# Kernel optimization log

Measured on AMD Instinct MI355X. Metric: run time of the kernel, lower is better.

## Reference

```python
import jax, jax.numpy as jnp
import numpy as np

TOP_K = 4  # num_experts_per_tok


def setup_inputs() -> dict:
    key = jax.random.key(0)
    ks = jax.random.split(key, 5)
    T, H, M, E = 2048, 1024, 512, 32
    sH = 1.0 / np.sqrt(H)
    sM = 1.0 / np.sqrt(M)
    return {
        "x": jax.random.normal(ks[0], (T, 1, H), dtype=jnp.float32),
        "gate_w": jax.random.normal(ks[1], (E, H), dtype=jnp.float32) * sH,   # router nn.Linear weight [E, H]
        "w_gate": jax.random.normal(ks[2], (E, M, H), dtype=jnp.float32) * sH,  # ffn_gate_exps, per expert [M, H]
        "w_up": jax.random.normal(ks[3], (E, M, H), dtype=jnp.float32) * sH,    # ffn_up_exps
        "w_down": jax.random.normal(ks[4], (E, H, M), dtype=jnp.float32) * sM,  # ffn_down_exps, per expert [H, M]
    }


def reference(x, gate_w, w_gate, w_up, w_down):
    # x: [T, S, H]; only the last position is used (decode path)
    curr = x[:, -1, :]                                   # [T, H]
    T = curr.shape[0]
    E = gate_w.shape[0]

    # router: logits = curr @ gate_w^T, top-k, softmax over top-k logits
    logits = curr @ gate_w.T                             # [T, E]
    topk_vals, topk_ids = jax.lax.top_k(logits, TOP_K)   # [T, K]
    topk_weights = jax.nn.softmax(topk_vals, axis=-1)    # [T, K]

    # dense routing matrix [T, E]: weight for chosen experts, 0 elsewhere
    route = jnp.zeros((T, E), dtype=curr.dtype)
    route = route.at[jnp.arange(T)[:, None], topk_ids].add(topk_weights)

    # expert MLPs: gate/up -> silu(gate)*up -> down, weighted combine
    gate_act = jnp.einsum('th,emh->tem', curr, w_gate)   # [T, E, M]
    up_act = jnp.einsum('th,emh->tem', curr, w_up)
    mixed = jax.nn.silu(gate_act) * up_act * route[:, :, None]
    out = jnp.einsum('tem,ehm->th', mixed, w_down)       # [T, H]

    return out.reshape(T, 1, -1)
```

## Files before the change

kernel.cpp:

```cpp
#include <hip/hip_runtime.h>
#include <math.h>

#define T_TOK 2048
#define H_DIM 1024
#define M_DIM 512
#define E_NUM 32
#define TOPK  4

#define BT  128
#define BK  32
#define GU_BM 64
#define DN_BH 128
#define MAX_TILES 96

typedef __bf16 bf16x8 __attribute__((ext_vector_type(8)));
typedef float f32x4 __attribute__((ext_vector_type(4)));
typedef unsigned short u16x8 __attribute__((ext_vector_type(8)));

__device__ __forceinline__ unsigned short f2bf(float f) {
  unsigned u = __float_as_uint(f);
  return (unsigned short)((u + 0x7fffu + ((u >> 16) & 1u)) >> 16);
}
__device__ __forceinline__ float bf2f(unsigned short h) {
  return __uint_as_float(((unsigned)h) << 16);
}
__device__ __forceinline__ f32x4 mfma16(bf16x8 a, bf16x8 b, f32x4 c) {
  return __builtin_amdgcn_mfma_f32_16x16x32_bf16(a, b, c, 0, 0, 0);
}

__global__ __launch_bounds__(512) void split_x_kernel(
    const float* __restrict__ x, unsigned short* __restrict__ xh,
    unsigned short* __restrict__ xl) {
  int i = (blockIdx.x * 512 + threadIdx.x) * 8;
  float t8[8];
  *(float4*)t8 = *(const float4*)(x + i);
  *(float4*)(t8 + 4) = *(const float4*)(x + i + 4);
  u16x8 hv, lv;
  #pragma unroll
  for (int j = 0; j < 8; ++j) {
    unsigned short h = f2bf(t8[j]);
    hv[j] = h;
    lv[j] = f2bf(t8[j] - bf2f(h));
  }
  *(u16x8*)(xh + i) = hv;
  *(u16x8*)(xl + i) = lv;
}

__global__ __launch_bounds__(256) void gating_kernel(
    const float* __restrict__ x, const float* __restrict__ gate_w,
    int* __restrict__ topk_ids, float* __restrict__ topk_w) {
  __shared__ float xr[H_DIM];
  __shared__ float logits[E_NUM];
  int t = blockIdx.x;
  int tid = threadIdx.x;
  const float* xrow = x + (size_t)t * H_DIM;
  *(float4*)(xr + tid * 4) = *(const float4*)(xrow + tid * 4);
  __syncthreads();
  int wave = tid >> 6, lane = tid & 63;
  const float4* x4 = (const float4*)xr;
  for (int e8 = 0; e8 < 8; ++e8) {
    int e = wave * 8 + e8;
    const float4* g4 = (const float4*)(gate_w + (size_t)e * H_DIM);
    float p = 0.f;
    #pragma unroll
    for (int i = 0; i < 4; ++i) {
      float4 a = x4[lane + i * 64];
      float4 b = g4[lane + i * 64];
      p += a.x * b.x + a.y * b.y + a.z * b.z + a.w * b.w;
    }
    for (int off = 32; off > 0; off >>= 1) p += __shfl_down(p, off, 64);
    if (lane == 0) logits[e] = p;
  }
  __syncthreads();
  if (tid == 0) {
    float v[E_NUM];
    for (int e = 0; e < E_NUM; ++e) v[e] = logits[e];
    int ids[TOPK]; float vals[TOPK];
    for (int k = 0; k < TOPK; ++k) {
      int bi = 0; float bv = -1e30f;
      for (int e = 0; e < E_NUM; ++e) if (v[e] > bv) { bv = v[e]; bi = e; }
      ids[k] = bi; vals[k] = bv; v[bi] = -1e30f;
    }
    float m = vals[0];
    float w[TOPK]; float s = 0.f;
    for (int k = 0; k < TOPK; ++k) { w[k] = expf(vals[k] - m); s += w[k]; }
    float inv = 1.f / s;
    for (int k = 0; k < TOPK; ++k) {
      topk_ids[t * TOPK + k] = ids[k];
      topk_w[t * TOPK + k]   = w[k] * inv;
    }
  }
}

__global__ __launch_bounds__(256) void scatter_kernel(
    const int* __restrict__ topk_ids, int* __restrict__ cursors,
    int* __restrict__ tok_list) {
  int g = blockIdx.x * 256 + threadIdx.x;
  if (g >= T_TOK * TOPK) return;
  int e = topk_ids[g];
  int slot = atomicAdd(&cursors[e], 1);
  tok_list[e * T_TOK + slot] = g;
}

__global__ void build_tiles(const int* __restrict__ cursors,
                            int* __restrict__ n_tiles, int* __restrict__ tile_list) {
  int lane = threadIdx.x;
  int nt = 0;
  if (lane < E_NUM) nt = (cursors[lane] + BT - 1) / BT;
  int pfx = nt;
  for (int off = 1; off < 64; off <<= 1) {
    int v = __shfl_up(pfx, off, 64);
    if (lane >= off) pfx += v;
  }
  int excl = pfx - nt;
  if (lane == E_NUM - 1) *n_tiles = pfx;
  if (lane < E_NUM)
    for (int i = 0; i < nt; ++i) tile_list[excl + i] = (lane << 8) | i;
}

__global__ __launch_bounds__(512) void gateup_mfma(
    const unsigned short* __restrict__ xh, const unsigned short* __restrict__ xl,
    const float* __restrict__ w_gate, const float* __restrict__ w_up,
    const float* __restrict__ topk_w,
    const int* __restrict__ cursors, const int* __restrict__ tok_list,
    const int* __restrict__ n_tiles, const int* __restrict__ tile_list,
    unsigned short* __restrict__ mixed) {
  if (blockIdx.y >= *n_tiles) return;
  int tid = threadIdx.x;
  int entry = tile_list[blockIdx.y];
  int e = entry >> 8, tile = entry & 255;
  int cnt = cursors[e];
  int m0 = blockIdx.x * GU_BM;

  __shared__ unsigned short Ah[BT * BK], Al[BT * BK];
  __shared__ unsigned short Gh[GU_BM * BK], Uh[GU_BM * BK];
  __shared__ int   ent[BT];
  __shared__ float rw[BT];

  if (tid < BT) {
    int idx = tile * BT + tid;
    int en = (idx < cnt) ? tok_list[e * T_TOK + idx] : -1;
    ent[tid] = en;
    rw[tid]  = (en >= 0) ? topk_w[en] : 0.f;
  }
  __syncthreads();

  int arow = tid >> 2, akq = tid & 3;
  int aen = ent[arow];
  if (aen < 0) aen = ent[0];
  const unsigned short* pAh = xh + (size_t)(aen >> 2) * H_DIM + akq * 8;
  const unsigned short* pAl = xl + (size_t)(aen >> 2) * H_DIM + akq * 8;
  int aoff = (arow >> 4) * 512 + akq * 128 + (arow & 15) * 8;

  int bslot = tid & 255;
  int brow = bslot >> 2, bkq = bslot & 3;
  const float* pB = ((tid < 256) ? w_gate : w_up) +
                    ((size_t)e * M_DIM + m0 + brow) * H_DIM + bkq * 8;
  unsigned short* Bdst = (tid < 256) ? Gh : Uh;
  int boff = (brow >> 4) * 512 + bkq * 128 + (brow & 15) * 8;

  int lane = tid & 63, wid = tid >> 6;
  int wr = (wid >> 1) * 32;
  int wc = (wid & 1) * 32;
  int l16 = lane * 8;

  f32x4 accg[2][2] = {}; f32x4 accu[2][2] = {};

  u16x8 rah, ral; float bf8[8];
  rah = *(const u16x8*)pAh;
  ral = *(const u16x8*)pAl;
  *(float4*)bf8 = *(const float4*)pB;
  *(float4*)(bf8 + 4) = *(const float4*)(pB + 4);

  const int NK = H_DIM / BK;
  for (int ks = 0; ks < NK; ++ks) {
    u16x8 bh;
    #pragma unroll
    for (int j = 0; j < 8; ++j) bh[j] = f2bf(bf8[j]);
    __syncthreads();
    *(u16x8*)&Ah[aoff] = rah;
    *(u16x8*)&Al[aoff] = ral;
    *(u16x8*)&Bdst[boff] = bh;
    __syncthreads();
    if (ks + 1 < NK) {
      int kq = (ks + 1) * BK;
      rah = *(const u16x8*)(pAh + kq);
      ral = *(const u16x8*)(pAl + kq);
      *(float4*)bf8 = *(const float4*)(pB + kq);
      *(float4*)(bf8 + 4) = *(const float4*)(pB + kq + 4);
    }
    int ab = (wr >> 4) * 512 + l16;
    bf16x8 a0h = *(const bf16x8*)&Ah[ab];
    bf16x8 a1h = *(const bf16x8*)&Ah[ab + 512];
    bf16x8 a0l = *(const bf16x8*)&Al[ab];
    bf16x8 a1l = *(const bf16x8*)&Al[ab + 512];
    #pragma unroll
    for (int nf = 0; nf < 2; ++nf) {
      int nb = ((wc >> 4) + nf) * 512 + l16;
      bf16x8 g = *(const bf16x8*)&Gh[nb];
      bf16x8 u = *(const bf16x8*)&Uh[nb];
      accg[0][nf] = mfma16(a0h, g, accg[0][nf]);
      accg[0][nf] = mfma16(a0l, g, accg[0][nf]);
      accg[1][nf] = mfma16(a1h, g, accg[1][nf]);
      accg[1][nf] = mfma16(a1l, g, accg[1][nf]);
      accu[0][nf] = mfma16(a0h, u, accu[0][nf]);
      accu[0][nf] = mfma16(a0l, u, accu[0][nf]);
      accu[1][nf] = mfma16(a1h, u, accu[1][nf]);
      accu[1][nf] = mfma16(a1l, u, accu[1][nf]);
    }
  }

  #pragma unroll
  for (int mf = 0; mf < 2; ++mf) {
    #pragma unroll
    for (int j = 0; j < 4; ++j) {
      int tr = wr + mf * 16 + (lane >> 4) * 4 + j;
      int en = ent[tr];
      if (en < 0) continue;
      float w = rw[tr];
      #pragma unroll
      for (int nf = 0; nf < 2; ++nf) {
        float g = accg[mf][nf][j], u = accu[mf][nf][j];
        float val = (g / (1.f + __expf(-g))) * u * w;
        mixed[(size_t)en * M_DIM + m0 + wc + nf * 16 + (lane & 15)] = f2bf(val);
      }
    }
  }
}

__global__ __launch_bounds__(512) void down_mfma(
    const float* __restrict__ w_down, const unsigned short* __restrict__ mixed,
    const int* __restrict__ cursors, const int* __restrict__ tok_list,
    const int* __restrict__ n_tiles, const int* __restrict__ tile_list,
    float* __restrict__ out) {
  if (blockIdx.y >= *n_tiles) return;
  int tid = threadIdx.x;
  int entry = tile_list[blockIdx.y];
  int e = entry >> 8, tile = entry & 255;
  int cnt = cursors[e];
  int h0 = blockIdx.x * DN_BH;

  __shared__ unsigned short As[BT * BK];
  __shared__ unsigned short Bs[DN_BH * BK];
  __shared__ int ent[BT];

  if (tid < BT) {
    int idx = tile * BT + tid;
    ent[tid] = (idx < cnt) ? tok_list[e * T_TOK + idx] : -1;
  }
  __syncthreads();

  int arow = tid >> 2, akq = tid & 3;
  int aen = ent[arow];
  if (aen < 0) aen = ent[0];
  const unsigned short* pA = mixed + (size_t)aen * M_DIM + akq * 8;
  int aoff = (arow >> 4) * 512 + akq * 128 + (arow & 15) * 8;

  const float* pB = w_down + ((size_t)e * H_DIM + h0 + arow) * M_DIM + akq * 8;

  int lane = tid & 63, wid = tid >> 6;
  int wr = (wid >> 1) * 32, wc = (wid & 1) * 64;
  int l16 = lane * 8;

  f32x4 acc[2][4] = {};
  u16x8 ra; float bf8[8];
  ra = *(const u16x8*)pA;
  *(float4*)bf8 = *(const float4*)pB;
  *(float4*)(bf8 + 4) = *(const float4*)(pB + 4);

  const int NK = M_DIM / BK;
  for (int ks = 0; ks < NK; ++ks) {
    u16x8 bh;
    #pragma unroll
    for (int j = 0; j < 8; ++j) bh[j] = f2bf(bf8[j]);
    __syncthreads();
    *(u16x8*)&As[aoff] = ra;
    *(u16x8*)&Bs[aoff] = bh;
    __syncthreads();
    if (ks + 1 < NK) {
      int kq = (ks + 1) * BK;
      ra = *(const u16x8*)(pA + kq);
      *(float4*)bf8 = *(const float4*)(pB + kq);
      *(float4*)(bf8 + 4) = *(const float4*)(pB + kq + 4);
    }
    int ab = (wr >> 4) * 512 + l16;
    bf16x8 a0 = *(const bf16x8*)&As[ab];
    bf16x8 a1 = *(const bf16x8*)&As[ab + 512];
    #pragma unroll
    for (int nf = 0; nf < 4; ++nf) {
      bf16x8 b = *(const bf16x8*)&Bs[((wc >> 4) + nf) * 512 + l16];
      acc[0][nf] = mfma16(a0, b, acc[0][nf]);
      acc[1][nf] = mfma16(a1, b, acc[1][nf]);
    }
  }

  #pragma unroll
  for (int mf = 0; mf < 2; ++mf) {
    #pragma unroll
    for (int j = 0; j < 4; ++j) {
      int tr = wr + mf * 16 + (lane >> 4) * 4 + j;
      int en = ent[tr];
      if (en < 0) continue;
      int t = en >> 2;
      #pragma unroll
      for (int nf = 0; nf < 4; ++nf)
        atomicAdd(&out[(size_t)t * H_DIM + h0 + wc + nf * 16 + (lane & 15)],
                  acc[mf][nf][j]);
    }
  }
}

extern "C" void kernel_launch(void* const* d_in, const int* in_sizes, int n_in,
                              void* d_out, int out_size, void* d_ws, size_t ws_size,
                              hipStream_t stream) {
  const float* x      = (const float*)d_in[0];
  const float* gate_w = (const float*)d_in[1];
  const float* w_gate = (const float*)d_in[2];
  const float* w_up   = (const float*)d_in[3];
  const float* w_down = (const float*)d_in[4];
  float* out = (float*)d_out;

  char* ws = (char*)d_ws;
  size_t off = 0;
  int*   topk_ids  = (int*)(ws + off);   off += (size_t)T_TOK * TOPK * 4;
  float* topk_w    = (float*)(ws + off); off += (size_t)T_TOK * TOPK * 4;
  int*   cursors   = (int*)(ws + off);   off += 256;
  int*   n_tiles   = (int*)(ws + off);   off += 64;
  int*   tile_list = (int*)(ws + off);   off += MAX_TILES * 4 + 64;
  int*   tok_list  = (int*)(ws + off);   off += (size_t)E_NUM * T_TOK * 4;
  unsigned short* x_hi  = (unsigned short*)(ws + off); off += (size_t)T_TOK * H_DIM * 2;
  unsigned short* x_lo  = (unsigned short*)(ws + off); off += (size_t)T_TOK * H_DIM * 2;
  unsigned short* mixed = (unsigned short*)(ws + off); off += (size_t)T_TOK * TOPK * M_DIM * 2;

  hipMemsetAsync(cursors, 0, E_NUM * sizeof(int), stream);
  hipMemsetAsync(out, 0, (size_t)T_TOK * H_DIM * sizeof(float), stream);

  split_x_kernel<<<T_TOK * H_DIM / (512 * 8), 512, 0, stream>>>(x, x_hi, x_lo);
  gating_kernel<<<T_TOK, 256, 0, stream>>>(x, gate_w, topk_ids, topk_w);
  scatter_kernel<<<(T_TOK * TOPK) / 256, 256, 0, stream>>>(topk_ids, cursors, tok_list);
  build_tiles<<<1, 64, 0, stream>>>(cursors, n_tiles, tile_list);
  gateup_mfma<<<dim3(M_DIM / GU_BM, MAX_TILES), 512, 0, stream>>>(
      x_hi, x_lo, w_gate, w_up, topk_w, cursors, tok_list, n_tiles, tile_list, mixed);
  down_mfma<<<dim3(H_DIM / DN_BH, MAX_TILES), 512, 0, stream>>>(
      w_down, mixed, cursors, tok_list, n_tiles, tile_list, out);
}
```

Before: 163.1 us.

## Double-buffer LDS in MoE GEMMs and fuse split/scatter into gating

Fuses the bf16 hi/lo split of x and the expert scatter into the gating kernel, removing two kernel launches and the topk_ids round trip through global memory. Both gate/up and down MFMA kernels now double-buffer their LDS tiles, so the next tile is written while the current one is consumed, and they use one lightweight barrier per K step instead of two. The LDS store layout becomes a linear per-thread offset. LDS use doubles, which may lower occupancy, and the atomic scatter now happens serially on one thread per token block.

```diff
diff --git a/kernel.cpp b/kernel.cpp
--- a/kernel.cpp
+++ b/kernel.cpp
@@ -16,6 +16,7 @@
 typedef __bf16 bf16x8 __attribute__((ext_vector_type(8)));
 typedef float f32x4 __attribute__((ext_vector_type(4)));
 typedef unsigned short u16x8 __attribute__((ext_vector_type(8)));
+typedef unsigned short u16x4 __attribute__((ext_vector_type(4)));
 
 __device__ __forceinline__ unsigned short f2bf(float f) {
   unsigned u = __float_as_uint(f);
@@ -27,34 +28,37 @@
 __device__ __forceinline__ f32x4 mfma16(bf16x8 a, bf16x8 b, f32x4 c) {
   return __builtin_amdgcn_mfma_f32_16x16x32_bf16(a, b, c, 0, 0, 0);
 }
-
-__global__ __launch_bounds__(512) void split_x_kernel(
-    const float* __restrict__ x, unsigned short* __restrict__ xh,
-    unsigned short* __restrict__ xl) {
-  int i = (blockIdx.x * 512 + threadIdx.x) * 8;
-  float t8[8];
-  *(float4*)t8 = *(const float4*)(x + i);
-  *(float4*)(t8 + 4) = *(const float4*)(x + i + 4);
-  u16x8 hv, lv;
-  #pragma unroll
-  for (int j = 0; j < 8; ++j) {
-    unsigned short h = f2bf(t8[j]);
-    hv[j] = h;
-    lv[j] = f2bf(t8[j] - bf2f(h));
-  }
-  *(u16x8*)(xh + i) = hv;
-  *(u16x8*)(xl + i) = lv;
+__device__ __forceinline__ void soft_barrier() {
+  asm volatile("s_waitcnt lgkmcnt(0)" ::: "memory");
+  __builtin_amdgcn_sched_barrier(0);
+  __builtin_amdgcn_s_barrier();
+  __builtin_amdgcn_sched_barrier(0);
 }
 
 __global__ __launch_bounds__(256) void gating_kernel(
     const float* __restrict__ x, const float* __restrict__ gate_w,
-    int* __restrict__ topk_ids, float* __restrict__ topk_w) {
+    unsigned short* __restrict__ xh, unsigned short* __restrict__ xl,
+    float* __restrict__ topk_w, int* __restrict__ cursors,
+    int* __restrict__ tok_list) {
   __shared__ float xr[H_DIM];
   __shared__ float logits[E_NUM];
   int t = blockIdx.x;
   int tid = threadIdx.x;
   const float* xrow = x + (size_t)t * H_DIM;
-  *(float4*)(xr + tid * 4) = *(const float4*)(xrow + tid * 4);
+  float4 v = *(const float4*)(xrow + tid * 4);
+  *(float4*)(xr + tid * 4) = v;
+  {
+    float f[4] = {v.x, v.y, v.z, v.w};
+    u16x4 hv, lv;
+    #pragma unroll
+    for (int j = 0; j < 4; ++j) {
+      unsigned short h = f2bf(f[j]);
+      hv[j] = h;
+      lv[j] = f2bf(f[j] - bf2f(h));
+    }
+    *(u16x4*)(xh + (size_t)t * H_DIM + tid * 4) = hv;
+    *(u16x4*)(xl + (size_t)t * H_DIM + tid * 4) = lv;
+  }
   __syncthreads();
   int wave = tid >> 6, lane = tid & 63;
   const float4* x4 = (const float4*)xr;
@@ -73,33 +77,25 @@
   }
   __syncthreads();
   if (tid == 0) {
-    float v[E_NUM];
-    for (int e = 0; e < E_NUM; ++e) v[e] = logits[e];
+    float vv[E_NUM];
+    for (int e = 0; e < E_NUM; ++e) vv[e] = logits[e];
     int ids[TOPK]; float vals[TOPK];
     for (int k = 0; k < TOPK; ++k) {
       int bi = 0; float bv = -1e30f;
-      for (int e = 0; e < E_NUM; ++e) if (v[e] > bv) { bv = v[e]; bi = e; }
-      ids[k] = bi; vals[k] = bv; v[bi] = -1e30f;
+      for (int e = 0; e < E_NUM; ++e) if (vv[e] > bv) { bv = vv[e]; bi = e; }
+      ids[k] = bi; vals[k] = bv; vv[bi] = -1e30f;
     }
     float m = vals[0];
     float w[TOPK]; float s = 0.f;
     for (int k = 0; k < TOPK; ++k) { w[k] = expf(vals[k] - m); s += w[k]; }
     float inv = 1.f / s;
     for (int k = 0; k < TOPK; ++k) {
-      topk_ids[t * TOPK + k] = ids[k];
-      topk_w[t * TOPK + k]   = w[k] * inv;
-    }
-  }
-}
-
-__global__ __launch_bounds__(256) void scatter_kernel(
-    const int* __restrict__ topk_ids, int* __restrict__ cursors,
-    int* __restrict__ tok_list) {
-  int g = blockIdx.x * 256 + threadIdx.x;
-  if (g >= T_TOK * TOPK) return;
-  int e = topk_ids[g];
-  int slot = atomicAdd(&cursors[e], 1);
-  tok_list[e * T_TOK + slot] = g;
+      int g = t * TOPK + k;
+      topk_w[g] = w[k] * inv;
+      int slot = atomicAdd(&cursors[ids[k]], 1);
+      tok_list[ids[k] * T_TOK + slot] = g;
+    }
+  }
 }
 
 __global__ void build_tiles(const int* __restrict__ cursors,
@@ -132,8 +128,8 @@
   int cnt = cursors[e];
   int m0 = blockIdx.x * GU_BM;
 
-  __shared__ unsigned short Ah[BT * BK], Al[BT * BK];
-  __shared__ unsigned short Gh[GU_BM * BK], Uh[GU_BM * BK];
+  __shared__ unsigned short Ah[2][BT * BK], Al[2][BT * BK];
+  __shared__ unsigned short Gh[2][GU_BM * BK], Uh[2][GU_BM * BK];
   __shared__ int   ent[BT];
   __shared__ float rw[BT];
 
@@ -145,19 +141,20 @@
   }
   __syncthreads();
 
-  int arow = tid >> 2, akq = tid & 3;
+  int arow = ((tid >> 6) << 4) + (tid & 15);
+  int akq  = (tid >> 4) & 3;
   int aen = ent[arow];
   if (aen < 0) aen = ent[0];
   const unsigned short* pAh = xh + (size_t)(aen >> 2) * H_DIM + akq * 8;
   const unsigned short* pAl = xl + (size_t)(aen >> 2) * H_DIM + akq * 8;
-  int aoff = (arow >> 4) * 512 + akq * 128 + (arow & 15) * 8;
+  int aoff = tid * 8;
 
   int bslot = tid & 255;
-  int brow = bslot >> 2, bkq = bslot & 3;
+  int brow = (((bslot >> 6) & 3) << 4) + (bslot & 15);
+  int bkq  = (bslot >> 4) & 3;
   const float* pB = ((tid < 256) ? w_gate : w_up) +
                     ((size_t)e * M_DIM + m0 + brow) * H_DIM + bkq * 8;
-  unsigned short* Bdst = (tid < 256) ? Gh : Uh;
-  int boff = (brow >> 4) * 512 + bkq * 128 + (brow & 15) * 8;
+  int boff = bslot * 8;
 
   int lane = tid & 63, wid = tid >> 6;
   int wr = (wid >> 1) * 32;
@@ -171,43 +168,71 @@
   ral = *(const u16x8*)pAl;
   *(float4*)bf8 = *(const float4*)pB;
   *(float4*)(bf8 + 4) = *(const float4*)(pB + 4);
+  {
+    u16x8 bh;
+    #pragma unroll
+    for (int j = 0; j < 8; ++j) bh[j] = f2bf(bf8[j]);
+    *(u16x8*)&Ah[0][aoff] = rah;
+    *(u16x8*)&Al[0][aoff] = ral;
+    if (tid < 256) *(u16x8*)&Gh[0][boff] = bh;
+    else           *(u16x8*)&Uh[0][boff] = bh;
+  }
+  __syncthreads();
+  rah = *(const u16x8*)(pAh + BK);
+  ral = *(const u16x8*)(pAl + BK);
+  *(float4*)bf8 = *(const float4*)(pB + BK);
+  *(float4*)(bf8 + 4) = *(const float4*)(pB + BK + 4);
 
   const int NK = H_DIM / BK;
+  int cur = 0;
   for (int ks = 0; ks < NK; ++ks) {
-    u16x8 bh;
-    #pragma unroll
-    for (int j = 0; j < 8; ++j) bh[j] = f2bf(bf8[j]);
-    __syncthreads();
-    *(u16x8*)&Ah[aoff] = rah;
-    *(u16x8*)&Al[aoff] = ral;
-    *(u16x8*)&Bdst[boff] = bh;
-    __syncthreads();
+    int ab = (wr >> 4) * 512 + l16;
+    bf16x8 a0h = *(const bf16x8*)&Ah[cur][ab];
+    bf16x8 a1h = *(const bf16x8*)&Ah[cur][ab + 512];
+    bf16x8 a0l = *(const bf16x8*)&Al[cur][ab];
+    bf16x8 a1l = *(const bf16x8*)&Al[cur][ab + 512];
+    int nb0 = (wc >> 4) * 512 + l16;
+    bf16x8 g0 = *(const bf16x8*)&Gh[cur][nb0];
+    bf16x8 g1 = *(const bf16x8*)&Gh[cur][nb0 + 512];
+    bf16x8 u0 = *(const bf16x8*)&Uh[cur][nb0];
+    bf16x8 u1 = *(const bf16x8*)&Uh[cur][nb0 + 512];
+
     if (ks + 1 < NK) {
-      int kq = (ks + 1) * BK;
-      rah = *(const u16x8*)(pAh + kq);
-      ral = *(const u16x8*)(pAl + kq);
-      *(float4*)bf8 = *(const float4*)(pB + kq);
-      *(float4*)(bf8 + 4) = *(const float4*)(pB + kq + 4);
-    }
-    int ab = (wr >> 4) * 512 + l16;
-    bf16x8 a0h = *(const bf16x8*)&Ah[ab];
-    bf16x8 a1h = *(const bf16x8*)&Ah[ab + 512];
-    bf16x8 a0l = *(const bf16x8*)&Al[ab];
-    bf16x8 a1l = *(const bf16x8*)&Al[ab + 512];
-    #pragma unroll
-    for (int nf = 0; nf < 2; ++nf) {
-      int nb = ((wc >> 4) + nf) * 512 + l16;
-      bf16x8 g = *(const bf16x8*)&Gh[nb];
-      bf16x8 u = *(const bf16x8*)&Uh[nb];
-      accg[0][nf] = mfma16(a0h, g, accg[0][nf]);
-      accg[0][nf] = mfma16(a0l, g, accg[0][nf]);
-      accg[1][nf] = mfma16(a1h, g, accg[1][nf]);
-      accg[1][nf] = mfma16(a1l, g, accg[1][nf]);
-      accu[0][nf] = mfma16(a0h, u, accu[0][nf]);
-      accu[0][nf] = mfma16(a0l, u, accu[0][nf]);
-      accu[1][nf] = mfma16(a1h, u, accu[1][nf]);
-      accu[1][nf] = mfma16(a1l, u, accu[1][nf]);
-    }
+      u16x8 bh;
+      #pragma unroll
+      for (int j = 0; j < 8; ++j) bh[j] = f2bf(bf8[j]);
+      *(u16x8*)&Ah[cur ^ 1][aoff] = rah;
+      *(u16x8*)&Al[cur ^ 1][aoff] = ral;
+      if (tid < 256) *(u16x8*)&Gh[cur ^ 1][boff] = bh;
+      else           *(u16x8*)&Uh[cur ^ 1][boff] = bh;
+      if (ks + 2 < NK) {
+        int kq = (ks + 2) * BK;
+        rah = *(const u16x8*)(pAh + kq);
+        ral = *(const u16x8*)(pAl + kq);
+        *(float4*)bf8 = *(const float4*)(pB + kq);
+        *(float4*)(bf8 + 4) = *(const float4*)(pB + kq + 4);
+      }
+    }
+
+    accg[0][0] = mfma16(a0h, g0, accg[0][0]);
+    accg[0][0] = mfma16(a0l, g0, accg[0][0]);
+    accg[1][0] = mfma16(a1h, g0, accg[1][0]);
+    accg[1][0] = mfma16(a1l, g0, accg[1][0]);
+    accg[0][1] = mfma16(a0h, g1, accg[0][1]);
+    accg[0][1] = mfma16(a0l, g1, accg[0][1]);
+    accg[1][1] = mfma16(a1h, g1, accg[1][1]);
+    accg[1][1] = mfma16(a1l, g1, accg[1][1]);
+    accu[0][0] = mfma16(a0h, u0, accu[0][0]);
+    accu[0][0] = mfma16(a0l, u0, accu[0][0]);
+    accu[1][0] = mfma16(a1h, u0, accu[1][0]);
+    accu[1][0] = mfma16(a1l, u0, accu[1][0]);
+    accu[0][1] = mfma16(a0h, u1, accu[0][1]);
+    accu[0][1] = mfma16(a0l, u1, accu[0][1]);
+    accu[1][1] = mfma16(a1h, u1, accu[1][1]);
+    accu[1][1] = mfma16(a1l, u1, accu[1][1]);
+
+    if (ks + 1 < NK) soft_barrier();
+    cur ^= 1;
   }
 
   #pragma unroll
@@ -240,8 +265,8 @@
   int cnt = cursors[e];
   int h0 = blockIdx.x * DN_BH;
 
-  __shared__ unsigned short As[BT * BK];
-  __shared__ unsigned short Bs[DN_BH * BK];
+  __shared__ unsigned short As[2][BT * BK];
+  __shared__ unsigned short Bs[2][DN_BH * BK];
   __shared__ int ent[BT];
 
   if (tid < BT) {
@@ -250,13 +275,13 @@
   }
   __syncthreads();
 
-  int arow = tid >> 2, akq = tid & 3;
+  int arow = ((tid >> 6) << 4) + (tid & 15);
+  int akq  = (tid >> 4) & 3;
   int aen = ent[arow];
   if (aen < 0) aen = ent[0];
   const unsigned short* pA = mixed + (size_t)aen * M_DIM + akq * 8;
-  int aoff = (arow >> 4) * 512 + akq * 128 + (arow & 15) * 8;
-
   const float* pB = w_down + ((size_t)e * H_DIM + h0 + arow) * M_DIM + akq * 8;
+  int soff = tid * 8;
 
   int lane = tid & 63, wid = tid >> 6;
   int wr = (wid >> 1) * 32, wc = (wid & 1) * 64;
@@ -267,31 +292,54 @@
   ra = *(const u16x8*)pA;
   *(float4*)bf8 = *(const float4*)pB;
   *(float4*)(bf8 + 4) = *(const float4*)(pB + 4);
+  {
+    u16x8 bh;
+    #pragma unroll
+    for (int j = 0; j < 8; ++j) bh[j] = f2bf(bf8[j]);
+    *(u16x8*)&As[0][soff] = ra;
+    *(u16x8*)&Bs[0][soff] = bh;
+  }
+  __syncthreads();
+  ra = *(const u16x8*)(pA + BK);
+  *(float4*)bf8 = *(const float4*)(pB + BK);
+  *(float4*)(bf8 + 4) = *(const float4*)(pB + BK + 4);
 
   const int NK = M_DIM / BK;
+  int cur = 0;
   for (int ks = 0; ks < NK; ++ks) {
-    u16x8 bh;
-    #pragma unroll
-    for (int j = 0; j < 8; ++j) bh[j] = f2bf(bf8[j]);
-    __syncthreads();
-    *(u16x8*)&As[aoff] = ra;
-    *(u16x8*)&Bs[aoff] = bh;
-    __syncthreads();
+    int ab = (wr >> 4) * 512 + l16;
+    bf16x8 a0 = *(const bf16x8*)&As[cur][ab];
+    bf16x8 a1 = *(const bf16x8*)&As[cur][ab + 512];
+    bf16x8 b0 = *(const bf16x8*)&Bs[cur][((wc >> 4) + 0) * 512 + l16];
+    bf16x8 b1 = *(const bf16x8*)&Bs[cur][((wc >> 4) + 1) * 512 + l16];
+    bf16x8 b2 = *(const bf16x8*)&Bs[cur][((wc >> 4) + 2) * 512 + l16];
+    bf16x8 b3 = *(const bf16x8*)&Bs[cur][((wc >> 4) + 3) * 512 + l16];
+
     if (ks + 1 < NK) {
-      int kq = (ks + 1) * BK;
-      ra = *(const u16x8*)(pA + kq);
-      *(float4*)bf8 = *(const float4*)(pB + kq);
-      *(float4*)(bf8 + 4) = *(const float4*)(pB + kq + 4);
-    }
-    int ab = (wr >> 4) * 512 + l16;
-    bf16x8 a0 = *(const bf16x8*)&As[ab];
-    bf16x8 a1 = *(const bf16x8*)&As[ab + 512];
-    #pragma unroll
-    for (int nf = 0; nf < 4; ++nf) {
-      bf16x8 b = *(const bf16x8*)&Bs[((wc >> 4) + nf) * 512 + l16];
-      acc[0][nf] = mfma16(a0, b, acc[0][nf]);
-      acc[1][nf] = mfma16(a1, b, acc[1][nf]);
-    }
+      u16x8 bh;
+      #pragma unroll
+      for (int j = 0; j < 8; ++j) bh[j] = f2bf(bf8[j]);
+      *(u16x8*)&As[cur ^ 1][soff] = ra;
+      *(u16x8*)&Bs[cur ^ 1][soff] = bh;
+      if (ks + 2 < NK) {
+        int kq = (ks + 2) * BK;
+        ra = *(const u16x8*)(pA + kq);
+        *(float4*)bf8 = *(const float4*)(pB + kq);
+        *(float4*)(bf8 + 4) = *(const float4*)(pB + kq + 4);
+      }
+    }
+
+    acc[0][0] = mfma16(a0, b0, acc[0][0]);
+    acc[1][0] = mfma16(a1, b0, acc[1][0]);
+    acc[0][1] = mfma16(a0, b1, acc[0][1]);
+    acc[1][1] = mfma16(a1, b1, acc[1][1]);
+    acc[0][2] = mfma16(a0, b2, acc[0][2]);
+    acc[1][2] = mfma16(a1, b2, acc[1][2]);
+    acc[0][3] = mfma16(a0, b3, acc[0][3]);
+    acc[1][3] = mfma16(a1, b3, acc[1][3]);
+
+    if (ks + 1 < NK) soft_barrier();
+    cur ^= 1;
   }
 
   #pragma unroll
@@ -322,7 +370,6 @@
 
   char* ws = (char*)d_ws;
   size_t off = 0;
-  int*   topk_ids  = (int*)(ws + off);   off += (size_t)T_TOK * TOPK * 4;
   float* topk_w    = (float*)(ws + off); off += (size_t)T_TOK * TOPK * 4;
   int*   cursors   = (int*)(ws + off);   off += 256;
   int*   n_tiles   = (int*)(ws + off);   off += 64;
@@ -335,9 +382,8 @@
   hipMemsetAsync(cursors, 0, E_NUM * sizeof(int), stream);
   hipMemsetAsync(out, 0, (size_t)T_TOK * H_DIM * sizeof(float), stream);
 
-  split_x_kernel<<<T_TOK * H_DIM / (512 * 8), 512, 0, stream>>>(x, x_hi, x_lo);
-  gating_kernel<<<T_TOK, 256, 0, stream>>>(x, gate_w, topk_ids, topk_w);
-  scatter_kernel<<<(T_TOK * TOPK) / 256, 256, 0, stream>>>(topk_ids, cursors, tok_list);
+  gating_kernel<<<T_TOK, 256, 0, stream>>>(x, gate_w, x_hi, x_lo, topk_w,
+                                           cursors, tok_list);
   build_tiles<<<1, 64, 0, stream>>>(cursors, n_tiles, tile_list);
   gateup_mfma<<<dim3(M_DIM / GU_BM, MAX_TILES), 512, 0, stream>>>(
       x_hi, x_lo, w_gate, w_up, topk_w, cursors, tok_list, n_tiles, tile_list, mixed);
```

Result: slower. 234.0 us (+43.4%).

## Fuse split and scatter into gating; halve token tile and double-buffer registers

Applied to the files above, without the earlier changes.

Folds the x hi/lo bf16 split and the expert-scatter atomics into the gating kernel, which removes two kernel launches and one extra pass over x. The token tile shrinks from 128 to 64 with 256-thread blocks and more tiles (MAX_TILES 160), so fewer padded rows are wasted per expert and more blocks run in parallel. Each thread now loads two K-steps of global data into alternating register sets, so the next loads overlap the current compute. The cost is more weight reloads per token and extra register pressure, and the per-expert token order now depends on atomics issued by a single thread per token.

```diff
diff --git a/kernel.cpp b/kernel.cpp
--- a/kernel.cpp
+++ b/kernel.cpp
@@ -7,15 +7,16 @@
 #define E_NUM 32
 #define TOPK  4
 
-#define BT  128
-#define BK  32
+#define BT    64
+#define BK    32
 #define GU_BM 64
 #define DN_BH 128
-#define MAX_TILES 96
+#define MAX_TILES 160
 
 typedef __bf16 bf16x8 __attribute__((ext_vector_type(8)));
 typedef float f32x4 __attribute__((ext_vector_type(4)));
 typedef unsigned short u16x8 __attribute__((ext_vector_type(8)));
+typedef unsigned short u16x4 __attribute__((ext_vector_type(4)));
 
 __device__ __forceinline__ unsigned short f2bf(float f) {
   unsigned u = __float_as_uint(f);
@@ -28,33 +29,30 @@
   return __builtin_amdgcn_mfma_f32_16x16x32_bf16(a, b, c, 0, 0, 0);
 }
 
-__global__ __launch_bounds__(512) void split_x_kernel(
-    const float* __restrict__ x, unsigned short* __restrict__ xh,
-    unsigned short* __restrict__ xl) {
-  int i = (blockIdx.x * 512 + threadIdx.x) * 8;
-  float t8[8];
-  *(float4*)t8 = *(const float4*)(x + i);
-  *(float4*)(t8 + 4) = *(const float4*)(x + i + 4);
-  u16x8 hv, lv;
-  #pragma unroll
-  for (int j = 0; j < 8; ++j) {
-    unsigned short h = f2bf(t8[j]);
-    hv[j] = h;
-    lv[j] = f2bf(t8[j] - bf2f(h));
-  }
-  *(u16x8*)(xh + i) = hv;
-  *(u16x8*)(xl + i) = lv;
-}
-
 __global__ __launch_bounds__(256) void gating_kernel(
     const float* __restrict__ x, const float* __restrict__ gate_w,
-    int* __restrict__ topk_ids, float* __restrict__ topk_w) {
+    unsigned short* __restrict__ xh, unsigned short* __restrict__ xl,
+    float* __restrict__ topk_w, int* __restrict__ cursors,
+    int* __restrict__ tok_list) {
   __shared__ float xr[H_DIM];
   __shared__ float logits[E_NUM];
   int t = blockIdx.x;
   int tid = threadIdx.x;
   const float* xrow = x + (size_t)t * H_DIM;
-  *(float4*)(xr + tid * 4) = *(const float4*)(xrow + tid * 4);
+  float4 v = *(const float4*)(xrow + tid * 4);
+  *(float4*)(xr + tid * 4) = v;
+  {
+    float f[4] = {v.x, v.y, v.z, v.w};
+    u16x4 hv, lv;
+    #pragma unroll
+    for (int j = 0; j < 4; ++j) {
+      unsigned short h = f2bf(f[j]);
+      hv[j] = h;
+      lv[j] = f2bf(f[j] - bf2f(h));
+    }
+    *(u16x4*)(xh + (size_t)t * H_DIM + tid * 4) = hv;
+    *(u16x4*)(xl + (size_t)t * H_DIM + tid * 4) = lv;
+  }
   __syncthreads();
   int wave = tid >> 6, lane = tid & 63;
   const float4* x4 = (const float4*)xr;
@@ -73,33 +71,25 @@
   }
   __syncthreads();
   if (tid == 0) {
-    float v[E_NUM];
-    for (int e = 0; e < E_NUM; ++e) v[e] = logits[e];
+    float vv[E_NUM];
+    for (int e = 0; e < E_NUM; ++e) vv[e] = logits[e];
     int ids[TOPK]; float vals[TOPK];
     for (int k = 0; k < TOPK; ++k) {
       int bi = 0; float bv = -1e30f;
-      for (int e = 0; e < E_NUM; ++e) if (v[e] > bv) { bv = v[e]; bi = e; }
-      ids[k] = bi; vals[k] = bv; v[bi] = -1e30f;
+      for (int e = 0; e < E_NUM; ++e) if (vv[e] > bv) { bv = vv[e]; bi = e; }
+      ids[k] = bi; vals[k] = bv; vv[bi] = -1e30f;
     }
     float m = vals[0];
     float w[TOPK]; float s = 0.f;
     for (int k = 0; k < TOPK; ++k) { w[k] = expf(vals[k] - m); s += w[k]; }
     float inv = 1.f / s;
     for (int k = 0; k < TOPK; ++k) {
-      topk_ids[t * TOPK + k] = ids[k];
-      topk_w[t * TOPK + k]   = w[k] * inv;
-    }
-  }
-}
-
-__global__ __launch_bounds__(256) void scatter_kernel(
-    const int* __restrict__ topk_ids, int* __restrict__ cursors,
-    int* __restrict__ tok_list) {
-  int g = blockIdx.x * 256 + threadIdx.x;
-  if (g >= T_TOK * TOPK) return;
-  int e = topk_ids[g];
-  int slot = atomicAdd(&cursors[e], 1);
-  tok_list[e * T_TOK + slot] = g;
+      int g = t * TOPK + k;
+      topk_w[g] = w[k] * inv;
+      int slot = atomicAdd(&cursors[ids[k]], 1);
+      tok_list[ids[k] * T_TOK + slot] = g;
+    }
+  }
 }
 
 __global__ void build_tiles(const int* __restrict__ cursors,
@@ -118,7 +108,7 @@
     for (int i = 0; i < nt; ++i) tile_list[excl + i] = (lane << 8) | i;
 }
 
-__global__ __launch_bounds__(512) void gateup_mfma(
+__global__ __launch_bounds__(256) void gateup_mfma(
     const unsigned short* __restrict__ xh, const unsigned short* __restrict__ xl,
     const float* __restrict__ w_gate, const float* __restrict__ w_up,
     const float* __restrict__ topk_w,
@@ -133,7 +123,7 @@
   int m0 = blockIdx.x * GU_BM;
 
   __shared__ unsigned short Ah[BT * BK], Al[BT * BK];
-  __shared__ unsigned short Gh[GU_BM * BK], Uh[GU_BM * BK];
+  __shared__ unsigned short Gs[GU_BM * BK], Us[GU_BM * BK];
   __shared__ int   ent[BT];
   __shared__ float rw[BT];
 
@@ -145,69 +135,84 @@
   }
   __syncthreads();
 
-  int arow = tid >> 2, akq = tid & 3;
-  int aen = ent[arow];
+  int srow = ((tid >> 6) << 4) + (tid & 15);
+  int skq  = (tid >> 4) & 3;
+  int aen = ent[srow];
   if (aen < 0) aen = ent[0];
-  const unsigned short* pAh = xh + (size_t)(aen >> 2) * H_DIM + akq * 8;
-  const unsigned short* pAl = xl + (size_t)(aen >> 2) * H_DIM + akq * 8;
-  int aoff = (arow >> 4) * 512 + akq * 128 + (arow & 15) * 8;
-
-  int bslot = tid & 255;
-  int brow = bslot >> 2, bkq = bslot & 3;
-  const float* pB = ((tid < 256) ? w_gate : w_up) +
-                    ((size_t)e * M_DIM + m0 + brow) * H_DIM + bkq * 8;
-  unsigned short* Bdst = (tid < 256) ? Gh : Uh;
-  int boff = (brow >> 4) * 512 + bkq * 128 + (brow & 15) * 8;
+  const unsigned short* pAh = xh + (size_t)(aen >> 2) * H_DIM + skq * 8;
+  const unsigned short* pAl = xl + (size_t)(aen >> 2) * H_DIM + skq * 8;
+  const float* pG = w_gate + ((size_t)e * M_DIM + m0 + srow) * H_DIM + skq * 8;
+  const float* pU = w_up   + ((size_t)e * M_DIM + m0 + srow) * H_DIM + skq * 8;
+  int soff = tid * 8;
 
   int lane = tid & 63, wid = tid >> 6;
   int wr = (wid >> 1) * 32;
   int wc = (wid & 1) * 32;
-  int l16 = lane * 8;
+  int l8 = lane * 8;
 
   f32x4 accg[2][2] = {}; f32x4 accu[2][2] = {};
 
-  u16x8 rah, ral; float bf8[8];
-  rah = *(const u16x8*)pAh;
-  ral = *(const u16x8*)pAl;
-  *(float4*)bf8 = *(const float4*)pB;
-  *(float4*)(bf8 + 4) = *(const float4*)(pB + 4);
-
+  u16x8 rah0, ral0, rah1, ral1;
+  float rg0[8], ru0[8], rg1[8], ru1[8];
+
+#define GU_LOAD(S, k0_) { \
+    rah##S = *(const u16x8*)(pAh + (k0_)); \
+    ral##S = *(const u16x8*)(pAl + (k0_)); \
+    *(float4*)(rg##S)     = *(const float4*)(pG + (k0_)); \
+    *(float4*)(rg##S + 4) = *(const float4*)(pG + (k0_) + 4); \
+    *(float4*)(ru##S)     = *(const float4*)(pU + (k0_)); \
+    *(float4*)(ru##S + 4) = *(const float4*)(pU + (k0_) + 4); }
+
+#define GU_STORE(S) { \
+    u16x8 gq, uq; \
+    _Pragma("unroll") \
+    for (int j = 0; j < 8; ++j) { gq[j] = f2bf(rg##S[j]); uq[j] = f2bf(ru##S[j]); } \
+    *(u16x8*)&Ah[soff] = rah##S; \
+    *(u16x8*)&Al[soff] = ral##S; \
+    *(u16x8*)&Gs[soff] = gq; \
+    *(u16x8*)&Us[soff] = uq; }
+
+#define GU_COMPUTE() { \
+    int ab = (wr >> 4) * 512 + l8; \
+    bf16x8 a0h = *(const bf16x8*)&Ah[ab]; \
+    bf16x8 a1h = *(const bf16x8*)&Ah[ab + 512]; \
+    bf16x8 a0l = *(const bf16x8*)&Al[ab]; \
+    bf16x8 a1l = *(const bf16x8*)&Al[ab + 512]; \
+    int nb = (wc >> 4) * 512 + l8; \
+    bf16x8 g0 = *(const bf16x8*)&Gs[nb]; \
+    bf16x8 g1 = *(const bf16x8*)&Gs[nb + 512]; \
+    bf16x8 u0 = *(const bf16x8*)&Us[nb]; \
+    bf16x8 u1 = *(const bf16x8*)&Us[nb + 512]; \
+    accg[0][0] = mfma16(a0h, g0, accg[0][0]); \
+    accg[0][0] = mfma16(a0l, g0, accg[0][0]); \
+    accg[1][0] = mfma16(a1h, g0, accg[1][0]); \
+    accg[1][0] = mfma16(a1l, g0, accg[1][0]); \
+    accg[0][1] = mfma16(a0h, g1, accg[0][1]); \
+    accg[0][1] = mfma16(a0l, g1, accg[0][1]); \
+    accg[1][1] = mfma16(a1h, g1, accg[1][1]); \
+    accg[1][1] = mfma16(a1l, g1, accg[1][1]); \
+    accu[0][0] = mfma16(a0h, u0, accu[0][0]); \
+    accu[0][0] = mfma16(a0l, u0, accu[0][0]); \
+    accu[1][0] = mfma16(a1h, u0, accu[1][0]); \
+    accu[1][0] = mfma16(a1l, u0, accu[1][0]); \
+    accu[0][1] = mfma16(a0h, u1, accu[0][1]); \
+    accu[0][1] = mfma16(a0l, u1, accu[0][1]); \
+    accu[1][1] = mfma16(a1h, u1, accu[1][1]); \
+    accu[1][1] = mfma16(a1l, u1, accu[1][1]); }
+
+  GU_LOAD(0, 0);
   const int NK = H_DIM / BK;
-  for (int ks = 0; ks < NK; ++ks) {
-    u16x8 bh;
-    #pragma unroll
-    for (int j = 0; j < 8; ++j) bh[j] = f2bf(bf8[j]);
-    __syncthreads();
-    *(u16x8*)&Ah[aoff] = rah;
-    *(u16x8*)&Al[aoff] = ral;
-    *(u16x8*)&Bdst[boff] = bh;
-    __syncthreads();
-    if (ks + 1 < NK) {
-      int kq = (ks + 1) * BK;
-      rah = *(const u16x8*)(pAh + kq);
-      ral = *(const u16x8*)(pAl + kq);
-      *(float4*)bf8 = *(const float4*)(pB + kq);
-      *(float4*)(bf8 + 4) = *(const float4*)(pB + kq + 4);
-    }
-    int ab = (wr >> 4) * 512 + l16;
-    bf16x8 a0h = *(const bf16x8*)&Ah[ab];
-    bf16x8 a1h = *(const bf16x8*)&Ah[ab + 512];
-    bf16x8 a0l = *(const bf16x8*)&Al[ab];
-    bf16x8 a1l = *(const bf16x8*)&Al[ab + 512];
-    #pragma unroll
-    for (int nf = 0; nf < 2; ++nf) {
-      int nb = ((wc >> 4) + nf) * 512 + l16;
-      bf16x8 g = *(const bf16x8*)&Gh[nb];
-      bf16x8 u = *(const bf16x8*)&Uh[nb];
-      accg[0][nf] = mfma16(a0h, g, accg[0][nf]);
-      accg[0][nf] = mfma16(a0l, g, accg[0][nf]);
-      accg[1][nf] = mfma16(a1h, g, accg[1][nf]);
-      accg[1][nf] = mfma16(a1l, g, accg[1][nf]);
-      accu[0][nf] = mfma16(a0h, u, accu[0][nf]);
-      accu[0][nf] = mfma16(a0l, u, accu[0][nf]);
-      accu[1][nf] = mfma16(a1h, u, accu[1][nf]);
-      accu[1][nf] = mfma16(a1l, u, accu[1][nf]);
-    }
+  for (int ks = 0; ks < NK; ks += 2) {
+    __syncthreads();
+    GU_LOAD(1, (ks + 1) * BK);
+    GU_STORE(0);
+    __syncthreads();
+    GU_COMPUTE();
+    __syncthreads();
+    if (ks + 2 < NK) GU_LOAD(0, (ks + 2) * BK);
+    GU_STORE(1);
+    __syncthreads();
+    GU_COMPUTE();
   }
 
   #pragma unroll
@@ -228,7 +233,7 @@
   }
 }
 
-__global__ __launch_bounds__(512) void down_mfma(
+__global__ __launch_bounds__(256) void down_mfma(
     const float* __restrict__ w_down, const unsigned short* __restrict__ mixed,
     const int* __restrict__ cursors, const int* __restrict__ tok_list,
     const int* __restrict__ n_tiles, const int* __restrict__ tile_list,
@@ -250,48 +255,70 @@
   }
   __syncthreads();
 
-  int arow = tid >> 2, akq = tid & 3;
-  int aen = ent[arow];
+  int srow = ((tid >> 6) << 4) + (tid & 15);
+  int skq  = (tid >> 4) & 3;
+  int aen = ent[srow];
   if (aen < 0) aen = ent[0];
-  const unsigned short* pA = mixed + (size_t)aen * M_DIM + akq * 8;
-  int aoff = (arow >> 4) * 512 + akq * 128 + (arow & 15) * 8;
-
-  const float* pB = w_down + ((size_t)e * H_DIM + h0 + arow) * M_DIM + akq * 8;
+  const unsigned short* pA = mixed + (size_t)aen * M_DIM + skq * 8;
+  const float* pB0 = w_down + ((size_t)e * H_DIM + h0 + srow) * M_DIM + skq * 8;
+  const float* pB1 = pB0 + (size_t)64 * M_DIM;
+  int soff = tid * 8;
 
   int lane = tid & 63, wid = tid >> 6;
-  int wr = (wid >> 1) * 32, wc = (wid & 1) * 64;
-  int l16 = lane * 8;
+  int wr = (wid >> 1) * 32;
+  int wc = (wid & 1) * 64;
+  int l8 = lane * 8;
 
   f32x4 acc[2][4] = {};
-  u16x8 ra; float bf8[8];
-  ra = *(const u16x8*)pA;
-  *(float4*)bf8 = *(const float4*)pB;
-  *(float4*)(bf8 + 4) = *(const float4*)(pB + 4);
-
+  u16x8 ra0, ra1;
+  float rb00[8], rb01[8], rb10[8], rb11[8];
+
+#define DN_LOAD(S, k0_) { \
+    ra##S = *(const u16x8*)(pA + (k0_)); \
+    *(float4*)(rb##S##0)     = *(const float4*)(pB0 + (k0_)); \
+    *(float4*)(rb##S##0 + 4) = *(const float4*)(pB0 + (k0_) + 4); \
+    *(float4*)(rb##S##1)     = *(const float4*)(pB1 + (k0_)); \
+    *(float4*)(rb##S##1 + 4) = *(const float4*)(pB1 + (k0_) + 4); }
+
+#define DN_STORE(S) { \
+    u16x8 b0q, b1q; \
+    _Pragma("unroll") \
+    for (int j = 0; j < 8; ++j) { b0q[j] = f2bf(rb##S##0[j]); b1q[j] = f2bf(rb##S##1[j]); } \
+    *(u16x8*)&As[soff] = ra##S; \
+    *(u16x8*)&Bs[soff] = b0q; \
+    *(u16x8*)&Bs[2048 + soff] = b1q; }
+
+#define DN_COMPUTE() { \
+    int ab = (wr >> 4) * 512 + l8; \
+    bf16x8 a0 = *(const bf16x8*)&As[ab]; \
+    bf16x8 a1 = *(const bf16x8*)&As[ab + 512]; \
+    int nb = (wc >> 4) * 512 + l8; \
+    bf16x8 b0 = *(const bf16x8*)&Bs[nb]; \
+    bf16x8 b1 = *(const bf16x8*)&Bs[nb + 512]; \
+    bf16x8 b2 = *(const bf16x8*)&Bs[nb + 1024]; \
+    bf16x8 b3 = *(const bf16x8*)&Bs[nb + 1536]; \
+    acc[0][0] = mfma16(a0, b0, acc[0][0]); \
+    acc[1][0] = mfma16(a1, b0, acc[1][0]); \
+    acc[0][1] = mfma16(a0, b1, acc[0][1]); \
+    acc[1][1] = mfma16(a1, b1, acc[1][1]); \
+    acc[0][2] = mfma16(a0, b2, acc[0][2]); \
+    acc[1][2] = mfma16(a1, b2, acc[1][2]); \
+    acc[0][3] = mfma16(a0, b3, acc[0][3]); \
+    acc[1][3] = mfma16(a1, b3, acc[1][3]); }
+
+  DN_LOAD(0, 0);
   const int NK = M_DIM / BK;
-  for (int ks = 0; ks < NK; ++ks) {
-    u16x8 bh;
-    #pragma unroll
-    for (int j = 0; j < 8; ++j) bh[j] = f2bf(bf8[j]);
-    __syncthreads();
-    *(u16x8*)&As[aoff] = ra;
-    *(u16x8*)&Bs[aoff] = bh;
-    __syncthreads();
-    if (ks + 1 < NK) {
-      int kq = (ks + 1) * BK;
-      ra = *(const u16x8*)(pA + kq);
-      *(float4*)bf8 = *(const float4*)(pB + kq);
-      *(float4*)(bf8 + 4) = *(const float4*)(pB + kq + 4);
-    }
-    int ab = (wr >> 4) * 512 + l16;
-    bf16x8 a0 = *(const bf16x8*)&As[ab];
-    bf16x8 a1 = *(const bf16x8*)&As[ab + 512];
-    #pragma unroll
-    for (int nf = 0; nf < 4; ++nf) {
-      bf16x8 b = *(const bf16x8*)&Bs[((wc >> 4) + nf) * 512 + l16];
-      acc[0][nf] = mfma16(a0, b, acc[0][nf]);
-      acc[1][nf] = mfma16(a1, b, acc[1][nf]);
-    }
+  for (int ks = 0; ks < NK; ks += 2) {
+    __syncthreads();
+    DN_LOAD(1, (ks + 1) * BK);
+    DN_STORE(0);
+    __syncthreads();
+    DN_COMPUTE();
+    __syncthreads();
+    if (ks + 2 < NK) DN_LOAD(0, (ks + 2) * BK);
+    DN_STORE(1);
+    __syncthreads();
+    DN_COMPUTE();
   }
 
   #pragma unroll
@@ -322,7 +349,6 @@
 
   char* ws = (char*)d_ws;
   size_t off = 0;
-  int*   topk_ids  = (int*)(ws + off);   off += (size_t)T_TOK * TOPK * 4;
   float* topk_w    = (float*)(ws + off); off += (size_t)T_TOK * TOPK * 4;
   int*   cursors   = (int*)(ws + off);   off += 256;
   int*   n_tiles   = (int*)(ws + off);   off += 64;
@@ -335,12 +361,11 @@
   hipMemsetAsync(cursors, 0, E_NUM * sizeof(int), stream);
   hipMemsetAsync(out, 0, (size_t)T_TOK * H_DIM * sizeof(float), stream);
 
-  split_x_kernel<<<T_TOK * H_DIM / (512 * 8), 512, 0, stream>>>(x, x_hi, x_lo);
-  gating_kernel<<<T_TOK, 256, 0, stream>>>(x, gate_w, topk_ids, topk_w);
-  scatter_kernel<<<(T_TOK * TOPK) / 256, 256, 0, stream>>>(topk_ids, cursors, tok_list);
+  gating_kernel<<<T_TOK, 256, 0, stream>>>(x, gate_w, x_hi, x_lo, topk_w,
+                                           cursors, tok_list);
   build_tiles<<<1, 64, 0, stream>>>(cursors, n_tiles, tile_list);
-  gateup_mfma<<<dim3(M_DIM / GU_BM, MAX_TILES), 512, 0, stream>>>(
+  gateup_mfma<<<dim3(M_DIM / GU_BM, MAX_TILES), 256, 0, stream>>>(
       x_hi, x_lo, w_gate, w_up, topk_w, cursors, tok_list, n_tiles, tile_list, mixed);
-  down_mfma<<<dim3(H_DIM / DN_BH, MAX_TILES), 512, 0, stream>>>(
+  down_mfma<<<dim3(H_DIM / DN_BH, MAX_TILES), 256, 0, stream>>>(
       w_down, mixed, cursors, tok_list, n_tiles, tile_list, out);
 }
```

After: 248.9 us. +52.6%, slower.
